# Optimization experiments

Measured on AMD Instinct MI355X. Metric: run time of the kernel, lower is better.

The kernel has to match this reference:

```python
import jax, jax.numpy as jnp
import numpy as np

B, S, D, H, DFF = 2, 2048, 1024, 16, 4096
DK = D // H
EPS = 1e-6


def setup_inputs() -> dict:
    key = jax.random.key(0)
    ks = jax.random.split(key, 16)
    sd = 0.02
    inp = {
        "x": jax.random.normal(ks[0], (B, S, D), jnp.float32),
        "mask": jnp.zeros((1, 1, S, S), jnp.float32),
        "wq": jax.random.normal(ks[1], (D, D), jnp.float32) * sd,
        "bq": jnp.zeros((D,), jnp.float32),
        "wk": jax.random.normal(ks[2], (D, D), jnp.float32) * sd,
        "bk": jnp.zeros((D,), jnp.float32),
        "wv": jax.random.normal(ks[3], (D, D), jnp.float32) * sd,
        "bv": jnp.zeros((D,), jnp.float32),
        "wo": jax.random.normal(ks[4], (D, D), jnp.float32) * sd,
        "bo": jnp.zeros((D,), jnp.float32),
        "w1": jax.random.normal(ks[5], (DFF, D), jnp.float32) * sd,
        "b1": jnp.zeros((DFF,), jnp.float32),
        "w2": jax.random.normal(ks[6], (D, DFF), jnp.float32) * sd,
        "b2": jnp.zeros((D,), jnp.float32),
        "alpha": jnp.ones((1,), jnp.float32),
        "gamma": jnp.zeros((1,), jnp.float32),
    }
    return inp


def _layer_norm(x, alpha, gamma):
    mean = jnp.mean(x, axis=-1, keepdims=True)
    var = jnp.mean((x - mean) ** 2, axis=-1, keepdims=True)
    return alpha * (x - mean) / jnp.sqrt(var + EPS) + gamma


def reference(x, mask, wq, bq, wk, bk, wv, bv, wo, bo, w1, b1, w2, b2, alpha, gamma):
    # --- multi-head attention (hand-rolled, full NxN scores) ---
    q = (x @ wq.T + bq).reshape(B, S, H, DK).transpose(0, 2, 1, 3)  # [B,H,S,DK]
    k = (x @ wk.T + bk).reshape(B, S, H, DK).transpose(0, 2, 1, 3)
    v = (x @ wv.T + bv).reshape(B, S, H, DK).transpose(0, 2, 1, 3)
    scores = jnp.einsum('bhqd,bhkd->bhqk', q, k) / np.sqrt(DK)  # [B,H,S,S]
    scores = scores + mask
    attn = jax.nn.softmax(scores, axis=-1)
    ctx = jnp.einsum('bhqk,bhkd->bhqd', attn, v)  # [B,H,S,DK]
    ctx = ctx.transpose(0, 2, 1, 3).reshape(B, S, D)
    attn_out = ctx @ wo.T + bo
    # residual + LayerNorm (dropout is identity in eval)
    out1 = _layer_norm(x + attn_out, alpha, gamma)
    # --- position-wise feed-forward ---
    ffn = jax.nn.relu(out1 @ w1.T + b1) @ w2.T + b2
    out2 = _layer_norm(out1 + ffn, alpha, gamma)
    return out2
```

## Files before the change

kernel.cpp:

```cpp
#include <hip/hip_runtime.h>


typedef float  f32x4   __attribute__((ext_vector_type(4)));
typedef float  f32x16  __attribute__((ext_vector_type(16)));
typedef __bf16 bf16x8  __attribute__((ext_vector_type(8)));
typedef __bf16 bf16x4  __attribute__((ext_vector_type(4)));

#define DEVI static __device__ __forceinline__

DEVI f32x4 mfma16(bf16x8 a, bf16x8 b, f32x4 c) {
    return __builtin_amdgcn_mfma_f32_16x16x32_bf16(a, b, c, 0, 0, 0);
}
DEVI f32x16 mfma32(bf16x8 a, bf16x8 b, f32x16 c) {
    return __builtin_amdgcn_mfma_f32_32x32x16_bf16(a, b, c, 0, 0, 0);
}

DEVI void gll16(const void* g, void* l) {
    __builtin_amdgcn_global_load_lds(
        (__attribute__((address_space(1))) void*)g,
        (__attribute__((address_space(3))) void*)l, 16, 0, 0);
}

DEVI __bf16 f2bf(float f) { return (__bf16)f; }

DEVI unsigned cvtpk_bf16(float a, float b) {
    unsigned d;
    asm("v_cvt_pk_bf16_f32 %0, %1, %2" : "=v"(d) : "v"(a), "v"(b));
    return d;
}
DEVI void permswap(unsigned& a, unsigned& b) {
    asm("v_permlane32_swap_b32 %0, %1" : "+v"(a), "+v"(b));
}
DEVI void permswapf(float& a, float& b) {
    asm("v_permlane32_swap_b32 %0, %1" : "+v"(a), "+v"(b));
}

__global__ void init_flag_kernel(int* f) { *f = 0; }

__global__ void mask_scan_kernel(const float* __restrict__ m, int* __restrict__ flag) {
    size_t i = (size_t)blockIdx.x * 256 + threadIdx.x;
    const float4* p = (const float4*)m;
    float4 a = p[i * 2], b = p[i * 2 + 1];
    bool nz = a.x != 0.f || a.y != 0.f || a.z != 0.f || a.w != 0.f ||
              b.x != 0.f || b.y != 0.f || b.z != 0.f || b.w != 0.f;
    if (__ballot(nz)) { if ((threadIdx.x & 63) == 0) atomicOr(flag, 1); }
}

__global__ void cast_bf16_kernel(const float* __restrict__ in, __bf16* __restrict__ out, int n8) {
    int i = blockIdx.x * 256 + threadIdx.x;
    if (i >= n8) return;
    const float4* p = (const float4*)in + (size_t)i * 2;
    float4 a = p[0], b = p[1];
    bf16x8 o = { (__bf16)a.x, (__bf16)a.y, (__bf16)a.z, (__bf16)a.w,
                 (__bf16)b.x, (__bf16)b.y, (__bf16)b.z, (__bf16)b.w };
    *(bf16x8*)(out + (size_t)i * 8) = o;
}

__global__ __launch_bounds__(256) void add_ln_kernel(
    const float* __restrict__ X, const float* __restrict__ Y,
    const float* __restrict__ alphap, const float* __restrict__ gammap,
    float* __restrict__ outF, __bf16* __restrict__ outB) {
    const int tid = threadIdx.x, lane = tid & 63, wid = tid >> 6;
    const size_t base = (size_t)blockIdx.x * 1024 + tid * 4;
    float4 xv = *(const float4*)&X[base];
    float4 yv = *(const float4*)&Y[base];
    float vx = xv.x + yv.x, vy = xv.y + yv.y, vz = xv.z + yv.z, vw = xv.w + yv.w;
    float s = vx + vy + vz + vw;
    #pragma unroll
    for (int o = 32; o; o >>= 1) s += __shfl_xor(s, o);
    __shared__ float red[4];
    if (lane == 0) red[wid] = s;
    __syncthreads();
    float mean = (red[0] + red[1] + red[2] + red[3]) * (1.0f / 1024.0f);
    float dx = vx - mean, dy = vy - mean, dz = vz - mean, dw = vw - mean;
    float s2 = dx * dx + dy * dy + dz * dz + dw * dw;
    #pragma unroll
    for (int o = 32; o; o >>= 1) s2 += __shfl_xor(s2, o);
    __syncthreads();
    if (lane == 0) red[wid] = s2;
    __syncthreads();
    float var = (red[0] + red[1] + red[2] + red[3]) * (1.0f / 1024.0f);
    float rstd = rsqrtf(var + 1e-6f);
    float a = alphap[0], g = gammap[0];
    float4 o4 = { a * dx * rstd + g, a * dy * rstd + g, a * dz * rstd + g, a * dw * rstd + g };
    *(float4*)&outF[base] = o4;
    if (outB) {
        bf16x4 ob = { f2bf(o4.x), f2bf(o4.y), f2bf(o4.z), f2bf(o4.w) };
        *(bf16x4*)&outB[base] = ob;
    }
}

template <int N, int K, int BN, int MODE>
__global__ __launch_bounds__(256, 2) void gemm_bt_kernel(
    const __bf16* __restrict__ A, const __bf16* __restrict__ W,
    const float* __restrict__ bias, void* __restrict__ outp) {
    constexpr int WN = BN / 2;
    constexpr int NI = WN / 16;
    __shared__ __bf16 lsA[128 * 64];
    __shared__ __bf16 lsB[BN * 64];
    const int tid = threadIdx.x, wid = tid >> 6, lane = tid & 63;
    const int wr = wid >> 1, wc = wid & 1, l15 = lane & 15, hi = lane >> 4;
    const int m0 = blockIdx.y * 128, n0 = blockIdx.x * BN;
    f32x4 acc[4][NI] = {};
    for (int kt = 0; kt < K / 64; ++kt) {
        #pragma unroll
        for (int i = 0; i < 4; ++i) {
            int row = wid * 32 + i * 8 + (lane >> 3);
            gll16(A + (size_t)(m0 + row) * K + kt * 64 + ((lane & 7) ^ (row & 7)) * 8,
                  &lsA[(wid * 32 + i * 8) * 64]);
        }
        #pragma unroll
        for (int i = 0; i < BN / 32; ++i) {
            int row = wid * (BN / 4) + i * 8 + (lane >> 3);
            gll16(W + (size_t)(n0 + row) * K + kt * 64 + ((lane & 7) ^ (row & 7)) * 8,
                  &lsB[(wid * (BN / 4) + i * 8) * 64]);
        }
        __syncthreads();
        #pragma unroll
        for (int s = 0; s < 2; ++s) {
            bf16x8 af[4], bfv[NI];
            #pragma unroll
            for (int mi = 0; mi < 4; ++mi) {
                int row = wr * 64 + mi * 16 + l15;
                af[mi] = *(const bf16x8*)&lsA[row * 64 + (((s * 4 + hi) ^ (row & 7)) * 8)];
            }
            #pragma unroll
            for (int ni = 0; ni < NI; ++ni) {
                int row = wc * WN + ni * 16 + l15;
                bfv[ni] = *(const bf16x8*)&lsB[row * 64 + (((s * 4 + hi) ^ (row & 7)) * 8)];
            }
            #pragma unroll
            for (int mi = 0; mi < 4; ++mi)
                #pragma unroll
                for (int ni = 0; ni < NI; ++ni)
                    acc[mi][ni] = mfma16(af[mi], bfv[ni], acc[mi][ni]);
        }
        __syncthreads();
    }
    #pragma unroll
    for (int ni = 0; ni < NI; ++ni) {
        int col = n0 + wc * WN + ni * 16 + l15;
        float bv = bias[col];
        #pragma unroll
        for (int mi = 0; mi < 4; ++mi) {
            int rowb = m0 + wr * 64 + mi * 16 + hi * 4;
            #pragma unroll
            for (int r = 0; r < 4; ++r) {
                float v = acc[mi][ni][r] + bv;
                if (MODE == 0) {
                    ((float*)outp)[(size_t)(rowb + r) * N + col] = v;
                } else {
                    v = fmaxf(v, 0.f);
                    ((__bf16*)outp)[(size_t)(rowb + r) * N + col] = f2bf(v);
                }
            }
        }
    }
}

__global__ __launch_bounds__(256, 2) void gemm_qkv_kernel(
    const __bf16* __restrict__ A,
    const __bf16* __restrict__ wq, const __bf16* __restrict__ wk, const __bf16* __restrict__ wv,
    const float* __restrict__ bq, const float* __restrict__ bk, const float* __restrict__ bv,
    __bf16* __restrict__ q, __bf16* __restrict__ k, __bf16* __restrict__ vt) {
    constexpr int K = 1024;
    const int z = blockIdx.z;
    const __bf16* W = (z == 0) ? wq : (z == 1) ? wk : wv;
    const float* bias = (z == 0) ? bq : (z == 1) ? bk : bv;
    __shared__ __bf16 lsA[128 * 64];
    __shared__ __bf16 lsB[128 * 64];
    const int tid = threadIdx.x, wid = tid >> 6, lane = tid & 63;
    const int wr = wid >> 1, wc = wid & 1, l15 = lane & 15, hi = lane >> 4;
    const int m0 = blockIdx.y * 128, n0 = blockIdx.x * 128;
    f32x4 acc[4][4] = {};
    for (int kt = 0; kt < K / 64; ++kt) {
        #pragma unroll
        for (int i = 0; i < 4; ++i) {
            int row = wid * 32 + i * 8 + (lane >> 3);
            gll16(A + (size_t)(m0 + row) * K + kt * 64 + ((lane & 7) ^ (row & 7)) * 8,
                  &lsA[(wid * 32 + i * 8) * 64]);
            gll16(W + (size_t)(n0 + row) * K + kt * 64 + ((lane & 7) ^ (row & 7)) * 8,
                  &lsB[(wid * 32 + i * 8) * 64]);
        }
        __syncthreads();
        #pragma unroll
        for (int s = 0; s < 2; ++s) {
            bf16x8 af[4], bfv[4];
            #pragma unroll
            for (int mi = 0; mi < 4; ++mi) {
                int row = wr * 64 + mi * 16 + l15;
                af[mi] = *(const bf16x8*)&lsA[row * 64 + (((s * 4 + hi) ^ (row & 7)) * 8)];
            }
            #pragma unroll
            for (int ni = 0; ni < 4; ++ni) {
                int row = wc * 64 + ni * 16 + l15;
                bfv[ni] = *(const bf16x8*)&lsB[row * 64 + (((s * 4 + hi) ^ (row & 7)) * 8)];
            }
            #pragma unroll
            for (int mi = 0; mi < 4; ++mi)
                #pragma unroll
                for (int ni = 0; ni < 4; ++ni)
                    acc[mi][ni] = mfma16(af[mi], bfv[ni], acc[mi][ni]);
        }
        __syncthreads();
    }
    const float scale = (z == 0) ? 0.125f * 1.4426950408889634f : 1.0f;
    #pragma unroll
    for (int ni = 0; ni < 4; ++ni) {
        int col = n0 + wc * 64 + ni * 16 + l15;
        int h = col >> 6, dk = col & 63;
        float bvv = bias[col];
        #pragma unroll
        for (int mi = 0; mi < 4; ++mi) {
            int rowb = m0 + wr * 64 + mi * 16 + hi * 4;
            int b_ = rowb >> 11, sb = rowb & 2047;
            if (z < 2) {
                __bf16* dst = (z == 0) ? q : k;
                #pragma unroll
                for (int r = 0; r < 4; ++r)
                    dst[((size_t)(b_ * 16 + h) * 2048 + sb + r) * 64 + dk] =
                        f2bf((acc[mi][ni][r] + bvv) * scale);
            } else {
                bf16x4 o = { f2bf(acc[mi][ni][0] + bvv), f2bf(acc[mi][ni][1] + bvv),
                             f2bf(acc[mi][ni][2] + bvv), f2bf(acc[mi][ni][3] + bvv) };
                *(bf16x4*)&vt[((size_t)(b_ * 16 + h) * 64 + dk) * 2048 + sb] = o;
            }
        }
    }
}

__global__ __launch_bounds__(256, 2) void flash_attn_kernel(
    const __bf16* __restrict__ Q, const __bf16* __restrict__ Kx,
    const __bf16* __restrict__ VT, const float* __restrict__ mask,
    const int* __restrict__ mflag, __bf16* __restrict__ ctx) {
    __shared__ __bf16 Kl[2][64 * 64];
    __shared__ __bf16 Vl[2][64 * 64];
    const int lane = threadIdx.x & 63, wid = threadIdx.x >> 6;
    const int l31 = lane & 31, h = lane >> 5;
    const int id = blockIdx.x;
    const int xcd = id & 7, rest = id >> 3;
    const int qt = rest & 15;
    const int bh = (rest >> 4) * 8 + xcd;
    const int q0 = qt * 128 + wid * 32;

    bf16x8 qf[4];
    const size_t qrow = (size_t)bh * 2048 + q0 + l31;
    #pragma unroll
    for (int st = 0; st < 4; ++st)
        qf[st] = *(const bf16x8*)&Q[qrow * 64 + st * 16 + h * 8];

    const __bf16* kbase = Kx + (size_t)bh * 2048 * 64;
    const __bf16* vbase = VT + (size_t)bh * 64 * 2048;

    f32x16 c0 = {}, c1 = {};
    f32x16 lv = {};
    const bool useMask = (*mflag != 0);

    const int r0 = wid * 16;
    const int rA = r0 + (lane >> 3);
    const int rB = rA + 8;
    const int cA = (lane & 7) ^ (rA & 7);
    const int cB = (lane & 7) ^ (rB & 7);

    auto stage = [&](int b, int t) {
        gll16(kbase + (size_t)(t * 64 + rA) * 64 + cA * 8, &Kl[b][r0 * 64]);
        gll16(kbase + (size_t)(t * 64 + rB) * 64 + cB * 8, &Kl[b][(r0 + 8) * 64]);
        gll16(vbase + (size_t)rA * 2048 + t * 64 + cA * 8, &Vl[b][r0 * 64]);
        gll16(vbase + (size_t)rB * 2048 + t * 64 + cB * 8, &Vl[b][(r0 + 8) * 64]);
    };

    stage(0, 0);
    __syncthreads();
    int cur = 0;

    for (int t = 0; t < 32; ++t) {
        const int tn = (t + 1 < 32) ? t + 1 : t;
        stage(cur ^ 1, tn);
        #pragma unroll
        for (int s = 0; s < 2; ++s) {
            const int krow = s * 32 + l31;
            f32x16 sc = {};
            __builtin_amdgcn_s_setprio(1);
            #pragma unroll
            for (int st = 0; st < 4; ++st) {
                bf16x8 kf = *(const bf16x8*)&Kl[cur][krow * 64 + (((st * 2 + h) ^ (krow & 7)) * 8)];
                sc = mfma32(kf, qf[st], sc);
            }
            __builtin_amdgcn_s_setprio(0);
            if (useMask) {
                #pragma unroll
                for (int r = 0; r < 16; ++r) {
                    int kv = t * 64 + s * 32 + (r & 3) + 8 * (r >> 2) + 4 * h;
                    sc[r] += mask[(size_t)(q0 + l31) * 2048 + kv] * 1.4426950408889634f;
                }
            }
            #pragma unroll
            for (int r = 0; r < 16; ++r) sc[r] = exp2f(sc[r] - 40.0f);
            lv += sc;
            unsigned w0 = cvtpk_bf16(sc[0], sc[1]),   w2 = cvtpk_bf16(sc[4], sc[5]);
            unsigned w1 = cvtpk_bf16(sc[2], sc[3]),   w3 = cvtpk_bf16(sc[6], sc[7]);
            permswap(w0, w2); permswap(w1, w3);
            unsigned w4 = cvtpk_bf16(sc[8], sc[9]),   w6 = cvtpk_bf16(sc[12], sc[13]);
            unsigned w5 = cvtpk_bf16(sc[10], sc[11]), w7 = cvtpk_bf16(sc[14], sc[15]);
            permswap(w4, w6); permswap(w5, w7);
            uint4 u0 = { w0, w1, w2, w3 }, u1 = { w4, w5, w6, w7 };
            bf16x8 pb0, pb1;
            __builtin_memcpy(&pb0, &u0, 16);
            __builtin_memcpy(&pb1, &u1, 16);
            const int vr0 = l31, vr1 = 32 + l31;
            bf16x8 v00 = *(const bf16x8*)&Vl[cur][vr0 * 64 + (((s * 4 + 0 + h) ^ (vr0 & 7)) * 8)];
            bf16x8 v01 = *(const bf16x8*)&Vl[cur][vr0 * 64 + (((s * 4 + 2 + h) ^ (vr0 & 7)) * 8)];
            bf16x8 v10 = *(const bf16x8*)&Vl[cur][vr1 * 64 + (((s * 4 + 0 + h) ^ (vr1 & 7)) * 8)];
            bf16x8 v11 = *(const bf16x8*)&Vl[cur][vr1 * 64 + (((s * 4 + 2 + h) ^ (vr1 & 7)) * 8)];
            __builtin_amdgcn_s_setprio(1);
            c0 = mfma32(v00, pb0, c0);
            c0 = mfma32(v01, pb1, c0);
            c1 = mfma32(v10, pb0, c1);
            c1 = mfma32(v11, pb1, c1);
            __builtin_amdgcn_s_setprio(0);
        }
        __syncthreads();
        cur ^= 1;
    }

    float y8[8], y4[4];
    #pragma unroll
    for (int r = 0; r < 8; ++r) y8[r] = lv[2 * r] + lv[2 * r + 1];
    #pragma unroll
    for (int r = 0; r < 4; ++r) y4[r] = y8[2 * r] + y8[2 * r + 1];
    float ls = (y4[0] + y4[1]) + (y4[2] + y4[3]);
    float la = ls, lb = ls;
    permswapf(la, lb);
    const float rinv = 1.0f / (la + lb);

    const int b_ = bh >> 4, h_ = bh & 15;
    const size_t obase = ((size_t)b_ * 2048 + q0 + l31) * 1024 + (size_t)h_ * 64;
    #pragma unroll
    for (int g = 0; g < 4; ++g) {
        bf16x4 o0 = { f2bf(c0[4 * g + 0] * rinv), f2bf(c0[4 * g + 1] * rinv),
                      f2bf(c0[4 * g + 2] * rinv), f2bf(c0[4 * g + 3] * rinv) };
        *(bf16x4*)&ctx[obase + g * 8 + h * 4] = o0;
        bf16x4 o1 = { f2bf(c1[4 * g + 0] * rinv), f2bf(c1[4 * g + 1] * rinv),
                      f2bf(c1[4 * g + 2] * rinv), f2bf(c1[4 * g + 3] * rinv) };
        *(bf16x4*)&ctx[obase + 32 + g * 8 + h * 4] = o1;
    }
}

extern "C" void kernel_launch(void* const* d_in, const int* in_sizes, int n_in,
                              void* d_out, int out_size, void* d_ws, size_t ws_size,
                              hipStream_t stream) {
    const float* x     = (const float*)d_in[0];
    const float* mask  = (const float*)d_in[1];
    const float* wq    = (const float*)d_in[2];
    const float* bq    = (const float*)d_in[3];
    const float* wk    = (const float*)d_in[4];
    const float* bk    = (const float*)d_in[5];
    const float* wv    = (const float*)d_in[6];
    const float* bv    = (const float*)d_in[7];
    const float* wo    = (const float*)d_in[8];
    const float* bo    = (const float*)d_in[9];
    const float* w1    = (const float*)d_in[10];
    const float* b1    = (const float*)d_in[11];
    const float* w2    = (const float*)d_in[12];
    const float* b2    = (const float*)d_in[13];
    const float* alpha = (const float*)d_in[14];
    const float* gamma = (const float*)d_in[15];

    char* ws = (char*)d_ws;
    const size_t MB = 1u << 20;
    __bf16* xb    = (__bf16*)(ws + 0 * MB);
    __bf16* qb    = (__bf16*)(ws + 8 * MB);
    __bf16* kb    = (__bf16*)(ws + 16 * MB);
    __bf16* vtb   = (__bf16*)(ws + 24 * MB);
    __bf16* ctxb  = (__bf16*)(ws + 32 * MB);
    __bf16* wqb   = (__bf16*)(ws + 40 * MB);
    __bf16* wkb   = (__bf16*)(ws + 42 * MB);
    __bf16* wvb   = (__bf16*)(ws + 44 * MB);
    __bf16* wob   = (__bf16*)(ws + 46 * MB);
    __bf16* w1b   = (__bf16*)(ws + 48 * MB);
    __bf16* w2b   = (__bf16*)(ws + 56 * MB);
    float*  attn  = (float*)(ws + 64 * MB);
    float*  out1  = (float*)(ws + 80 * MB);
    __bf16* out1b = (__bf16*)(ws + 96 * MB);
    __bf16* hid   = (__bf16*)(ws + 104 * MB);
    int*    mflag = (int*)(ws + 136 * MB);
    if (ws_size < 136 * MB + 64) return;

    init_flag_kernel<<<1, 1, 0, stream>>>(mflag);
    mask_scan_kernel<<<2048, 256, 0, stream>>>(mask, mflag);

    cast_bf16_kernel<<<2048, 256, 0, stream>>>(x, xb, 524288);
    cast_bf16_kernel<<<512, 256, 0, stream>>>(wq, wqb, 131072);
    cast_bf16_kernel<<<512, 256, 0, stream>>>(wk, wkb, 131072);
    cast_bf16_kernel<<<512, 256, 0, stream>>>(wv, wvb, 131072);
    cast_bf16_kernel<<<512, 256, 0, stream>>>(wo, wob, 131072);
    cast_bf16_kernel<<<2048, 256, 0, stream>>>(w1, w1b, 524288);
    cast_bf16_kernel<<<2048, 256, 0, stream>>>(w2, w2b, 524288);

    gemm_qkv_kernel<<<dim3(8, 32, 3), 256, 0, stream>>>(xb, wqb, wkb, wvb, bq, bk, bv,
                                                        qb, kb, vtb);
    flash_attn_kernel<<<dim3(512), 256, 0, stream>>>(qb, kb, vtb, mask, mflag, ctxb);
    gemm_bt_kernel<1024, 1024, 64, 0><<<dim3(16, 32), 256, 0, stream>>>(ctxb, wob, bo, attn);
    add_ln_kernel<<<4096, 256, 0, stream>>>(x, attn, alpha, gamma, out1, out1b);
    gemm_bt_kernel<4096, 1024, 128, 1><<<dim3(32, 32), 256, 0, stream>>>(out1b, w1b, b1, hid);
    gemm_bt_kernel<1024, 4096, 64, 0><<<dim3(16, 32), 256, 0, stream>>>(hid, w2b, b2, attn);
    add_ln_kernel<<<4096, 256, 0, stream>>>(out1, attn, alpha, gamma, (float*)d_out, nullptr);
}
```

Before: 272.2 us.

## Split attention KV range across two blocks and merge partial contexts

Each attention block now covers only half of the key/value tiles, doubling the grid to 1024 blocks. Each half writes unnormalised fp32 partial context and row sums to workspace, and a new merge kernel adds the halves, normalises and writes the bf16 context. The launch-bounds occupancy hint is raised from 2 to 4 blocks. The aim is more parallelism and better latency hiding on the attention stage, at the cost of extra fp32 round-trip traffic, one more launch and possible register pressure.

```diff
diff --git a/kernel.cpp b/kernel.cpp
--- a/kernel.cpp
+++ b/kernel.cpp
@@ -229,19 +229,22 @@
     }
 }
 
-__global__ __launch_bounds__(256, 2) void flash_attn_kernel(
+__global__ __launch_bounds__(256, 4) void flash_attn_kernel(
     const __bf16* __restrict__ Q, const __bf16* __restrict__ Kx,
     const __bf16* __restrict__ VT, const float* __restrict__ mask,
-    const int* __restrict__ mflag, __bf16* __restrict__ ctx) {
+    const int* __restrict__ mflag, float* __restrict__ ctxP,
+    float* __restrict__ lsum) {
     __shared__ __bf16 Kl[2][64 * 64];
     __shared__ __bf16 Vl[2][64 * 64];
     const int lane = threadIdx.x & 63, wid = threadIdx.x >> 6;
     const int l31 = lane & 31, h = lane >> 5;
     const int id = blockIdx.x;
     const int xcd = id & 7, rest = id >> 3;
-    const int qt = rest & 15;
-    const int bh = (rest >> 4) * 8 + xcd;
+    const int bh = xcd * 4 + (rest >> 5);
+    const int sub = rest & 31;
+    const int qt = sub >> 1, half = sub & 1;
     const int q0 = qt * 128 + wid * 32;
+    const int tbase = half * 16;
 
     bf16x8 qf[4];
     const size_t qrow = (size_t)bh * 2048 + q0 + l31;
@@ -269,12 +272,13 @@
         gll16(vbase + (size_t)rB * 2048 + t * 64 + cB * 8, &Vl[b][(r0 + 8) * 64]);
     };
 
-    stage(0, 0);
+    stage(0, tbase);
     __syncthreads();
     int cur = 0;
 
-    for (int t = 0; t < 32; ++t) {
-        const int tn = (t + 1 < 32) ? t + 1 : t;
+    for (int tt = 0; tt < 16; ++tt) {
+        const int t = tbase + tt;
+        const int tn = (tt + 1 < 16) ? t + 1 : t;
         stage(cur ^ 1, tn);
         #pragma unroll
         for (int s = 0; s < 2; ++s) {
@@ -331,19 +335,40 @@
     float ls = (y4[0] + y4[1]) + (y4[2] + y4[3]);
     float la = ls, lb = ls;
     permswapf(la, lb);
-    const float rinv = 1.0f / (la + lb);
-
+    const float lrow = la + lb;
+    if (h == 0) lsum[half * 65536 + bh * 2048 + q0 + l31] = lrow;
+
+    const size_t pbase = (size_t)half * 4194304 + ((size_t)bh * 2048 + q0 + l31) * 64;
+    #pragma unroll
+    for (int g = 0; g < 4; ++g) {
+        float4 o0 = { c0[4 * g + 0], c0[4 * g + 1], c0[4 * g + 2], c0[4 * g + 3] };
+        *(float4*)&ctxP[pbase + g * 8 + h * 4] = o0;
+        float4 o1 = { c1[4 * g + 0], c1[4 * g + 1], c1[4 * g + 2], c1[4 * g + 3] };
+        *(float4*)&ctxP[pbase + 32 + g * 8 + h * 4] = o1;
+    }
+}
+
+__global__ __launch_bounds__(256) void merge_ctx_kernel(
+    const float* __restrict__ ctxP, const float* __restrict__ lsum,
+    __bf16* __restrict__ ctx) {
+    const int idx = blockIdx.x * 256 + threadIdx.x;
+    const int oct = idx & 7;
+    const int q = (idx >> 3) & 2047;
+    const int bh = idx >> 14;
+    const size_t p0 = ((size_t)bh * 2048 + q) * 64 + oct * 8;
+    float4 a0 = *(const float4*)&ctxP[p0];
+    float4 a1 = *(const float4*)&ctxP[p0 + 4];
+    float4 b0 = *(const float4*)&ctxP[4194304 + p0];
+    float4 b1 = *(const float4*)&ctxP[4194304 + p0 + 4];
+    const float l = lsum[bh * 2048 + q] + lsum[65536 + bh * 2048 + q];
+    const float rinv = 1.0f / l;
     const int b_ = bh >> 4, h_ = bh & 15;
-    const size_t obase = ((size_t)b_ * 2048 + q0 + l31) * 1024 + (size_t)h_ * 64;
-    #pragma unroll
-    for (int g = 0; g < 4; ++g) {
-        bf16x4 o0 = { f2bf(c0[4 * g + 0] * rinv), f2bf(c0[4 * g + 1] * rinv),
-                      f2bf(c0[4 * g + 2] * rinv), f2bf(c0[4 * g + 3] * rinv) };
-        *(bf16x4*)&ctx[obase + g * 8 + h * 4] = o0;
-        bf16x4 o1 = { f2bf(c1[4 * g + 0] * rinv), f2bf(c1[4 * g + 1] * rinv),
-                      f2bf(c1[4 * g + 2] * rinv), f2bf(c1[4 * g + 3] * rinv) };
-        *(bf16x4*)&ctx[obase + 32 + g * 8 + h * 4] = o1;
-    }
+    const size_t o = ((size_t)b_ * 2048 + q) * 1024 + (size_t)h_ * 64 + oct * 8;
+    bf16x8 ov = { f2bf((a0.x + b0.x) * rinv), f2bf((a0.y + b0.y) * rinv),
+                  f2bf((a0.z + b0.z) * rinv), f2bf((a0.w + b0.w) * rinv),
+                  f2bf((a1.x + b1.x) * rinv), f2bf((a1.y + b1.y) * rinv),
+                  f2bf((a1.z + b1.z) * rinv), f2bf((a1.w + b1.w) * rinv) };
+    *(bf16x8*)&ctx[o] = ov;
 }
 
 extern "C" void kernel_launch(void* const* d_in, const int* in_sizes, int n_in,
@@ -384,6 +409,8 @@
     __bf16* out1b = (__bf16*)(ws + 96 * MB);
     __bf16* hid   = (__bf16*)(ws + 104 * MB);
     int*    mflag = (int*)(ws + 136 * MB);
+    float*  ctxP  = (float*)(ws + 104 * MB);
+    float*  lsumP = (float*)(ws + 96 * MB);
     if (ws_size < 136 * MB + 64) return;
 
     init_flag_kernel<<<1, 1, 0, stream>>>(mflag);
@@ -399,7 +426,8 @@
 
     gemm_qkv_kernel<<<dim3(8, 32, 3), 256, 0, stream>>>(xb, wqb, wkb, wvb, bq, bk, bv,
                                                         qb, kb, vtb);
-    flash_attn_kernel<<<dim3(512), 256, 0, stream>>>(qb, kb, vtb, mask, mflag, ctxb);
+    flash_attn_kernel<<<dim3(1024), 256, 0, stream>>>(qb, kb, vtb, mask, mflag, ctxP, lsumP);
+    merge_ctx_kernel<<<dim3(2048), 256, 0, stream>>>(ctxP, lsumP, ctxb);
     gemm_bt_kernel<1024, 1024, 64, 0><<<dim3(16, 32), 256, 0, stream>>>(ctxb, wob, bo, attn);
     add_ln_kernel<<<4096, 256, 0, stream>>>(x, attn, alpha, gamma, out1, out1b);
     gemm_bt_kernel<4096, 1024, 128, 1><<<dim3(32, 32), 256, 0, stream>>>(out1b, w1b, b1, hid);
```

New measurement: 284.7 us. 4.6% more time.
